# Kernel tuning notes

Hardware: AMD Instinct MI355X
Metric: run time of the kernel (lower is better)

The kernel has to match this reference:

```python
import jax, jax.numpy as jnp
import numpy as np
import math

B, T, C, NH, LEVEL = 2, 2048, 1024, 16, 3


def _build_sets(T, level):
    # hierarchical dyadic sets: levels `level`..floor(log2(T)), step 2^l
    sets = []
    levelmax = int(math.floor(math.log2(T)))
    for l in range(level, levelmax + 1):
        step = 2 ** l
        for i in range(T // step):
            sets.append((i * step, (i + 1) * step - 1))
    b = np.asarray(sets, dtype=np.int32)
    return b[:, 0], b[:, 1]


def setup_inputs() -> dict:
    key = jax.random.key(0)
    kx, kw1, kw2 = jax.random.split(key, 3)
    x = jax.random.normal(kx, (B, T, C), dtype=jnp.float32)
    # torch nn.Linear stores weight as (out_features, in_features); y = x @ W.T
    W_attn = jax.random.normal(kw1, (3 * C, C), dtype=jnp.float32) * (C ** -0.5)
    W_proj = jax.random.normal(kw2, (C, C), dtype=jnp.float32) * (C ** -0.5)
    return {"x": x, "W_attn": W_attn, "W_proj": W_proj}


def _get_slice(xc, l_idx, r_idx):
    # xc: (B,NH,T,hs) cumulative sums; returns sum over [l_idx, r_idx]
    r = xc[:, :, r_idx, :]
    l = xc[:, :, l_idx - 1, :] * (l_idx >= 1)[None, None, :, None].astype(xc.dtype)
    return r - l


def _forward(x, W_attn, W_proj):
    hs = C // NH
    scale = hs ** -0.5
    qkv = x @ W_attn.T                      # (B,T,3C)
    q, k, v = jnp.split(qkv, 3, axis=2)
    heads = lambda t: t.reshape(B, T, NH, hs).transpose(0, 2, 1, 3)  # (B,NH,T,hs)
    q, k, v = heads(q), heads(k), heads(v)
    phi = lambda t: jax.nn.elu(t) + 1.0     # feature_map = 'elu_plus'
    q_phi, k_phi = phi(q), phi(k)
    k_cum = jnp.cumsum(k_phi, axis=2)
    v_cum = jnp.cumsum(v, axis=2)

    l_np, r_np = _build_sets(T, LEVEL)
    l_idx, r_idx = jnp.asarray(l_np), jnp.asarray(r_np)
    K = _get_slice(k_cum, l_idx, r_idx)     # (B,NH,S,hs)
    V = _get_slice(v_cum, l_idx, r_idx)

    t_idx = jnp.arange(T)
    mask = t_idx[:, None] >= r_idx[None, :]                 # (T,S)
    logits = jnp.einsum('bhtd,bhsd->bhts', q, K) * scale    # raw q here (as in source)
    logits = jnp.where(mask[None, None], logits, -jnp.inf)

    # tail term over last (t mod 2^level)+1 tokens, uses q_phi
    Lmin = 2 ** LEVEL
    tail_len = t_idx % Lmin + 1
    l_tail = t_idx - tail_len + 1
    K_tail = _get_slice(k_cum, l_tail, t_idx)               # (B,NH,T,hs)
    V_tail = _get_slice(v_cum, l_tail, t_idx)
    tail_logit = jnp.sum(q_phi * K_tail, axis=-1) * scale   # (B,NH,T)

    full = jnp.concatenate([logits, tail_logit[..., None]], axis=-1)
    att = jax.nn.softmax(full, axis=-1)
    out = jnp.einsum('bhts,bhsd->bhtd', att[..., :-1], V) + att[..., -1:] * V_tail
    out = out.transpose(0, 2, 1, 3).reshape(B, T, C)
    return out @ W_proj.T


def reference(x, W_attn, W_proj):
    return _forward(x, W_attn, W_proj)
```

## Files before the change

### kernel.cpp

```cpp
#include <hip/hip_runtime.h>
#include <hip/hip_bf16.h>
#include <stdint.h>

#define B_    2
#define T_    2048
#define CD    1024
#define NH_   16
#define HS_   64
#define NSETS 511
#define NSP   512
#define QKV_LD 3072
#define NEGBIG (-3.4e38f)
#define QSC   (0.125f * 1.44269504088896f)

typedef __attribute__((ext_vector_type(8))) short  short8;
typedef __attribute__((ext_vector_type(4))) float  f32x4;
typedef _Float16 half8v __attribute__((ext_vector_type(8)));

__device__ __forceinline__ unsigned short f2bf(float f) {
  unsigned u = __float_as_uint(f);
  unsigned r = 0x7FFFu + ((u >> 16) & 1u);
  return (unsigned short)((u + r) >> 16);
}
__device__ __forceinline__ float bf2f(unsigned short h) {
  return __uint_as_float(((unsigned)h) << 16);
}
__device__ __forceinline__ unsigned short f2h(float v) {
  _Float16 h = (_Float16)v;
  return __builtin_bit_cast(unsigned short, h);
}
__device__ __forceinline__ float elu1(float x) {
  return x > 0.f ? x + 1.f : __expf(x);
}
__device__ __forceinline__ void gload16(const unsigned short* g, short* l) {
  __builtin_amdgcn_global_load_lds(
      (const __attribute__((address_space(1))) unsigned int*)g,
      (__attribute__((address_space(3))) unsigned int*)l, 16, 0, 0);
}

__global__ __launch_bounds__(256) void split3_kernel(
    const float* __restrict__ x, const float* __restrict__ Wa,
    const float* __restrict__ Wp,
    unsigned short* __restrict__ xh, unsigned short* __restrict__ xl,
    unsigned short* __restrict__ xf,
    unsigned short* __restrict__ waqh, unsigned short* __restrict__ waql,
    unsigned short* __restrict__ wakvf, unsigned short* __restrict__ wph) {
  int bid = blockIdx.x;
  int t = threadIdx.x;
  if (bid < 16384) {
    int i = bid * 256 + t;
    float v = x[i];
    unsigned short h = f2bf(v);
    xh[i] = h;
    xl[i] = f2bf(v - bf2f(h));
    xf[i] = f2h(v);
  } else if (bid < 20480) {
    int i = (bid - 16384) * 256 + t;
    float v = Wa[i];
    unsigned short h = f2bf(v);
    waqh[i] = h;
    waql[i] = f2bf(v - bf2f(h));
  } else if (bid < 28672) {
    int i = (bid - 20480) * 256 + t;
    wakvf[i] = f2h(Wa[1048576 + i]);
  } else {
    int i = (bid - 28672) * 256 + t;
    wph[i] = f2bf(Wp[i]);
  }
}

template<int SPLIT, int BN, int F16>
__device__ __forceinline__ void gemm_body(
    short* lds,
    const unsigned short* __restrict__ Ah, const unsigned short* __restrict__ Al,
    const unsigned short* __restrict__ Bh, const unsigned short* __restrict__ Bl,
    float* __restrict__ Cmat, int K, int ldc, int row0, int col0)
{
  constexpr int NB   = BN / 16;
  constexpr int ALD  = 8 * (1 + SPLIT);
  constexpr int TL   = ALD + NB * (1 + SPLIT);
  constexpr int PW   = TL / 4;
  constexpr int ASH  = (1 + SPLIT) * 4096;
  constexpr int ABYT = ASH * 2;
  constexpr int NC   = BN / 32;

  const int tid  = threadIdx.x;
  const int lane = tid & 63;
  const int w    = tid >> 6;
  const int wr   = w >> 1, wc = w & 1;

  f32x4 acc[4][NC];
  #pragma unroll
  for (int a = 0; a < 4; ++a)
    #pragma unroll
    for (int b = 0; b < NC; ++b)
      acc[a][b] = (f32x4){0.f, 0.f, 0.f, 0.f};

  const int rlane = lane & 15;
  const int kgrp  = lane >> 4;
  const int rsw   = (kgrp ^ (rlane & 3) ^ ((rlane >> 2) & 3)) << 4;

  const int slr = lane >> 2;
  const int sch = (lane & 3) ^ (slr & 3) ^ ((slr >> 2) & 3);

  for (int kt = 0; kt < K; kt += 32) {
    __syncthreads();
    #pragma unroll
    for (int li = 0; li < PW; ++li) {
      int L = w * PW + li;
      const unsigned short* src; int dsts; size_t rowb;
      if (L < 8)                { src = Ah; rowb = (size_t)row0 + L * 16;       dsts = L * 512; }
      else if (SPLIT && L < 16) { src = Al; rowb = (size_t)row0 + (L - 8) * 16; dsts = 4096 + (L - 8) * 512; }
      else {
        int Lb = L - ALD;
        if (!SPLIT || Lb < NB) { src = Bh; rowb = (size_t)col0 + Lb * 16;        dsts = ASH + Lb * 512; }
        else                   { src = Bl; rowb = (size_t)col0 + (Lb - NB) * 16; dsts = ASH + BN * 32 + (Lb - NB) * 512; }
      }
      gload16(src + (rowb + slr) * K + kt + (sch << 3), lds + dsts + lane * 8);
    }
    __syncthreads();

    short8 aH[4], bH[NC], aL[4], bL[NC];
    #pragma unroll
    for (int m = 0; m < 4; ++m) {
      int r = wr * 64 + m * 16 + rlane;
      aH[m] = *(const short8*)((const char*)lds + r * 64 + rsw);
      if (SPLIT) aL[m] = *(const short8*)((const char*)lds + 8192 + r * 64 + rsw);
    }
    #pragma unroll
    for (int n = 0; n < NC; ++n) {
      int c = wc * (BN / 2) + n * 16 + rlane;
      bH[n] = *(const short8*)((const char*)lds + ABYT + c * 64 + rsw);
      if (SPLIT) bL[n] = *(const short8*)((const char*)lds + ABYT + BN * 64 + c * 64 + rsw);
    }
    #pragma unroll
    for (int mm = 0; mm < 4; ++mm)
      #pragma unroll
      for (int nn = 0; nn < NC; ++nn) {
        if (F16) {
          acc[mm][nn] = __builtin_amdgcn_mfma_f32_16x16x32_f16(
              __builtin_bit_cast(half8v, aH[mm]), __builtin_bit_cast(half8v, bH[nn]),
              acc[mm][nn], 0, 0, 0);
        } else {
          acc[mm][nn] = __builtin_amdgcn_mfma_f32_16x16x32_bf16(aH[mm], bH[nn], acc[mm][nn], 0, 0, 0);
          if (SPLIT) {
            acc[mm][nn] = __builtin_amdgcn_mfma_f32_16x16x32_bf16(aH[mm], bL[nn], acc[mm][nn], 0, 0, 0);
            acc[mm][nn] = __builtin_amdgcn_mfma_f32_16x16x32_bf16(aL[mm], bH[nn], acc[mm][nn], 0, 0, 0);
          }
        }
      }
  }

  const int rl = (lane >> 4) * 4;
  const int cl = lane & 15;
  #pragma unroll
  for (int mm = 0; mm < 4; ++mm)
    #pragma unroll
    for (int nn = 0; nn < NC; ++nn)
      #pragma unroll
      for (int r = 0; r < 4; ++r) {
        int row = row0 + wr * 64 + mm * 16 + rl + r;
        int col = col0 + wc * (BN / 2) + nn * 16 + cl;
        Cmat[(size_t)row * ldc + col] = acc[mm][nn][r];
      }
}

template<int SPLIT, int BN, int F16>
__global__ __launch_bounds__(256) void gemm_bt(
    const unsigned short* __restrict__ Ah, const unsigned short* __restrict__ Al,
    const unsigned short* __restrict__ Bh, const unsigned short* __restrict__ Bl,
    float* __restrict__ Cmat, int M, int N, int K, int ldc)
{
  __shared__ short lds[(1 + SPLIT) * 4096 + (1 + SPLIT) * BN * 32];
  const int nwg = gridDim.x;
  const int cpx = nwg >> 3;
  const int bid = blockIdx.x;
  const int swb = (bid & 7) * cpx + (bid >> 3);
  const int nbx = N / BN;
  const int bx = swb % nbx;
  const int by = swb / nbx;
  gemm_body<SPLIT, BN, F16>(lds, Ah, Al, Bh, Bl, Cmat, K, ldc, by * 128, bx * BN);
}

__global__ __launch_bounds__(256) void cs_part(const float* __restrict__ qkv,
                                               float* __restrict__ part) {
  int blk = blockIdx.x;
  int q   = blk & 1;
  int seg = (blk >> 1) & 127;
  int b   = blk >> 8;
  int c   = threadIdx.x * 4;
  const float* src = qkv + (size_t)(b * T_ + seg * 16) * QKV_LD + CD + q * CD + c;
  float4 s = {0.f, 0.f, 0.f, 0.f};
  #pragma unroll 4
  for (int j = 0; j < 16; ++j) {
    float4 v = *(const float4*)(src + (size_t)j * QKV_LD);
    if (q == 0) {
      s.x += elu1(v.x); s.y += elu1(v.y); s.z += elu1(v.z); s.w += elu1(v.w);
    } else {
      s.x += v.x; s.y += v.y; s.z += v.z; s.w += v.w;
    }
  }
  *(float4*)(part + ((size_t)(b * 128 + seg) * 2048) + q * 1024 + c) = s;
}

__global__ __launch_bounds__(256) void cs_final(const float* __restrict__ qkv,
                                                const float* __restrict__ part,
                                                float* __restrict__ kcum,
                                                float* __restrict__ vcum) {
  int blk = blockIdx.x;
  int q   = blk & 1;
  int seg = (blk >> 1) & 127;
  int b   = blk >> 8;
  int c   = threadIdx.x * 4;
  int h   = c >> 6, d = c & 63;
  float4 s = {0.f, 0.f, 0.f, 0.f};
  const float* pb = part + (size_t)(b * 128) * 2048 + q * 1024 + c;
  #pragma unroll 8
  for (int ss = 0; ss < seg; ++ss) {
    float4 p = *(const float4*)(pb + (size_t)ss * 2048);
    s.x += p.x; s.y += p.y; s.z += p.z; s.w += p.w;
  }
  const float* src = qkv + (size_t)(b * T_ + seg * 16) * QKV_LD + CD + q * CD + c;
  float* dst = (q == 0 ? kcum : vcum) + ((size_t)(b * NH_ + h) * T_ + seg * 16) * HS_ + d;
  #pragma unroll 4
  for (int j = 0; j < 16; ++j) {
    float4 v = *(const float4*)(src + (size_t)j * QKV_LD);
    if (q == 0) {
      s.x += elu1(v.x); s.y += elu1(v.y); s.z += elu1(v.z); s.w += elu1(v.w);
    } else {
      s.x += v.x; s.y += v.y; s.z += v.z; s.w += v.w;
    }
    *(float4*)(dst + (size_t)j * HS_) = s;
  }
}

__global__ __launch_bounds__(256) void build_sets2(
    const float* __restrict__ kcum, const float* __restrict__ vcum,
    unsigned short* __restrict__ Ksh, unsigned short* __restrict__ Ksl,
    unsigned short* __restrict__ Vst, int* __restrict__ r_srt)
{
  __shared__ int   lr[64], lli[64];
  __shared__ float vt[64][65];
  const int bh = blockIdx.x >> 3;
  const int s0 = (blockIdx.x & 7) * 64;
  const int tid = threadIdx.x;

  for (int s = tid; s < NSP; s += 256) {
    int r, li, rank;
    if (s == NSETS) { r = 0x7fffffff; li = 0; rank = NSETS; }
    else {
      int lvl = 3, base = 0;
      while (s >= base + (T_ >> lvl)) { base += T_ >> lvl; ++lvl; }
      int i = s - base;
      int m = (i + 1) << lvl;
      r = m - 1; li = i << lvl;
      rank = lvl - 3;
      #pragma unroll
      for (int j = 3; j <= 11; ++j) rank += (m - 8) >> j;
    }
    if (rank >= s0 && rank < s0 + 64) {
      lr[rank - s0]  = r;
      lli[rank - s0] = li;
      if (bh == 0) r_srt[rank] = r;
    }
  }
  __syncthreads();

  const int sl = tid >> 2;
  const int dq = (tid & 3) * 16;
  const int r  = lr[sl], li = lli[sl];
  const size_t orow = ((size_t)(bh << 9) + s0 + sl) * HS_ + dq;
  short8 kh0, kh1, kl0, kl1;
  if (r == 0x7fffffff) {
    #pragma unroll
    for (int j = 0; j < 8; ++j) { kh0[j]=0; kh1[j]=0; kl0[j]=0; kl1[j]=0; }
    #pragma unroll
    for (int j = 0; j < 16; ++j) vt[sl][dq + j] = 0.f;
  } else {
    const float* kr0 = kcum + ((size_t)bh * T_ + r) * HS_ + dq;
    const float* vr0 = vcum + ((size_t)bh * T_ + r) * HS_ + dq;
    const float* kr1 = kcum + ((size_t)bh * T_ + (li - 1)) * HS_ + dq;
    const float* vr1 = vcum + ((size_t)bh * T_ + (li - 1)) * HS_ + dq;
    #pragma unroll
    for (int g = 0; g < 4; ++g) {
      float4 kv = *(const float4*)(kr0 + g * 4);
      float4 vv = *(const float4*)(vr0 + g * 4);
      if (li > 0) {
        float4 k1 = *(const float4*)(kr1 + g * 4);
        float4 v1 = *(const float4*)(vr1 + g * 4);
        kv.x -= k1.x; kv.y -= k1.y; kv.z -= k1.z; kv.w -= k1.w;
        vv.x -= v1.x; vv.y -= v1.y; vv.z -= v1.z; vv.w -= v1.w;
      }
      float ka[4] = {kv.x, kv.y, kv.z, kv.w};
      float va[4] = {vv.x, vv.y, vv.z, vv.w};
      #pragma unroll
      for (int j = 0; j < 4; ++j) {
        int e = g * 4 + j;
        unsigned short h = f2bf(ka[j]);
        unsigned short l = f2bf(ka[j] - bf2f(h));
        if (e < 8) { kh0[e] = (short)h; kl0[e] = (short)l; }
        else       { kh1[e - 8] = (short)h; kl1[e - 8] = (short)l; }
        vt[sl][dq + e] = va[j];
      }
    }
  }
  *(short8*)(Ksh + orow)     = kh0;
  *(short8*)(Ksh + orow + 8) = kh1;
  *(short8*)(Ksl + orow)     = kl0;
  *(short8*)(Ksl + orow + 8) = kl1;
  __syncthreads();

  const int d  = tid >> 2;
  const int sq = (tid & 3) * 16;
  short8 a, b2;
  #pragma unroll
  for (int j = 0; j < 8; ++j) {
    a[j]  = (short)f2bf(vt[sq + j][d]);
    b2[j] = (short)f2bf(vt[sq + 8 + j][d]);
  }
  unsigned short* dst = Vst + ((size_t)(bh << 6) + d) * NSP + s0 + sq;
  *(short8*)dst = a;
  *(short8*)(dst + 8) = b2;
}

__global__ __launch_bounds__(256) void attn_mfma(
    const float* __restrict__ qkv, const float* __restrict__ kcum,
    const float* __restrict__ vcum,
    const unsigned short* __restrict__ Ksh, const unsigned short* __restrict__ Ksl,
    const unsigned short* __restrict__ Vst, const int* __restrict__ r_srt,
    unsigned short* __restrict__ attnb)
{
  __shared__ short Pl[4 * 1024];
  __shared__ short KV[3 * 4096];
  __shared__ int   rs_lds[NSP];

  const int blk = blockIdx.x;
  const int xcd = blk & 7;
  const int j   = blk >> 3;
  const int bh  = xcd * 4 + (j >> 5);
  const int tch = (j + ((j >> 5) << 3)) & 31;
  const int b = bh >> 4, h = bh & 15;
  const int t0 = tch * 64;
  const int tid = threadIdx.x;
  const int lane = tid & 63;
  const int w = tid >> 6;
  const int col = lane & 15;
  const int kgrp = (lane >> 4) * 8;

  const int srow = lane >> 3;
  const int scsw = ((lane & 7) ^ srow) * 8;

  auto stage_tile = [&](int s0) {
    #pragma unroll
    for (int L = w * 6; L < w * 6 + 6; ++L) {
      int a = L >> 3, i = L & 7;
      const unsigned short* src;
      if (a == 0)      src = Ksh + ((size_t)(bh << 9) + s0 + i * 8 + srow) * 64 + scsw;
      else if (a == 1) src = Ksl + ((size_t)(bh << 9) + s0 + i * 8 + srow) * 64 + scsw;
      else             src = Vst + ((size_t)(bh << 6) + i * 8 + srow) * NSP + s0 + scsw;
      gload16(src, KV + a * 4096 + i * 512 + lane * 8);
    }
  };

  short8 qh[2], ql[2];
  {
    int qrow = t0 + w * 16 + col;
    const float* qr = qkv + (size_t)(b * T_ + qrow) * QKV_LD + h * HS_;
    #pragma unroll
    for (int ks = 0; ks < 2; ++ks) {
      float4 v0 = *(const float4*)(qr + kgrp + ks * 32);
      float4 v1 = *(const float4*)(qr + kgrp + ks * 32 + 4);
      float vv[8] = {v0.x, v0.y, v0.z, v0.w, v1.x, v1.y, v1.z, v1.w};
      #pragma unroll
      for (int jj = 0; jj < 8; ++jj) {
        float sv = vv[jj] * QSC;
        unsigned short hi = f2bf(sv);
        qh[ks][jj] = (short)hi;
        ql[ks][jj] = (short)f2bf(sv - bf2f(hi));
      }
    }
  }
  for (int s = tid; s < NSP; s += 256) rs_lds[s] = r_srt[s];

  int rows[4];
  #pragma unroll
  for (int r = 0; r < 4; ++r) rows[r] = t0 + w * 16 + (lane >> 4) * 4 + r;

  f32x4 O[4];
  float mrun[4], lsum[4];
  #pragma unroll
  for (int f = 0; f < 4; ++f) {
    O[f] = (f32x4){0.f, 0.f, 0.f, 0.f};
    mrun[f] = NEGBIG; lsum[f] = 0.f;
  }

  int nmax = 0;
  #pragma unroll
  for (int jj = 3; jj <= 11; ++jj) nmax += (t0 + 64) >> jj;
  const int ntiles = (nmax + 63) >> 6;

  for (int tile = 0; tile < ntiles; ++tile) {
    const int s0 = tile * 64;
    stage_tile(s0);
    __syncthreads();

    const char* kc = (const char*)KV;
    f32x4 S[4];
    #pragma unroll
    for (int f = 0; f < 4; ++f) S[f] = (f32x4){0.f, 0.f, 0.f, 0.f};

    #pragma unroll
    for (int ks = 0; ks < 2; ++ks) {
      int chnk = (lane >> 4) + ks * 4;
      #pragma unroll
      for (int f = 0; f < 4; ++f) {
        int so = f * 16 + col;
        int kb = so * 128 + ((chnk ^ (so & 7)) << 4);
        short8 bHv = *(const short8*)(kc + kb);
        short8 bLv = *(const short8*)(kc + 8192 + kb);
        S[f] = __builtin_amdgcn_mfma_f32_16x16x32_bf16(qh[ks], bHv, S[f], 0, 0, 0);
        S[f] = __builtin_amdgcn_mfma_f32_16x16x32_bf16(qh[ks], bLv, S[f], 0, 0, 0);
        S[f] = __builtin_amdgcn_mfma_f32_16x16x32_bf16(ql[ks], bHv, S[f], 0, 0, 0);
      }
    }

    int rsv[4];
    #pragma unroll
    for (int f = 0; f < 4; ++f) rsv[f] = rs_lds[s0 + f * 16 + col];

    float zv[4][4];
    #pragma unroll
    for (int f = 0; f < 4; ++f)
      #pragma unroll
      for (int r = 0; r < 4; ++r)
        zv[f][r] = (rsv[f] > rows[r]) ? NEGBIG : S[f][r];

    float mx[4];
    #pragma unroll
    for (int r = 0; r < 4; ++r)
      mx[r] = fmaxf(fmaxf(zv[0][r], zv[1][r]), fmaxf(zv[2][r], zv[3][r]));
    int pred = (mx[0] <= mrun[0] + 11.5f) & (mx[1] <= mrun[1] + 11.5f) &
               (mx[2] <= mrun[2] + 11.5f) & (mx[3] <= mrun[3] + 11.5f);
    if (!__all(pred)) {
      #pragma unroll
      for (int r = 0; r < 4; ++r) {
        float mt = mx[r];
        mt = fmaxf(mt, __shfl_xor(mt, 1));
        mt = fmaxf(mt, __shfl_xor(mt, 2));
        mt = fmaxf(mt, __shfl_xor(mt, 4));
        mt = fmaxf(mt, __shfl_xor(mt, 8));
        float mv = fmaxf(mrun[r], mt);
        float fs = exp2f(mrun[r] - mv);
        lsum[r] *= fs;
        #pragma unroll
        for (int f = 0; f < 4; ++f) O[f][r] *= fs;
        mrun[r] = mv;
      }
    }

    char* pw = (char*)Pl + w * 2048;
    #pragma unroll
    for (int r = 0; r < 4; ++r) {
      int rowr = (lane >> 4) * 4 + r;
      int rswz = (rowr & 7) << 4;
      #pragma unroll
      for (int f = 0; f < 4; ++f) {
        float p = exp2f(zv[f][r] - mrun[r]);
        p = (rsv[f] > rows[r]) ? 0.f : p;
        lsum[r] += p;
        int addr = (rowr * 128 + (f * 16 + col) * 2) ^ rswz;
        *(unsigned short*)(pw + addr) = f2bf(p);
      }
    }

    #pragma unroll
    for (int ks = 0; ks < 2; ++ks) {
      int chnk = (lane >> 4) + ks * 4;
      int pbyte = (col * 128 + (kgrp + ks * 32) * 2) ^ ((col & 7) << 4);
      short8 pa = *(const short8*)(pw + pbyte);
      #pragma unroll
      for (int f = 0; f < 4; ++f) {
        int dr = f * 16 + col;
        short8 bv = *(const short8*)(kc + 16384 + dr * 128 + ((chnk ^ (dr & 7)) << 4));
        O[f] = __builtin_amdgcn_mfma_f32_16x16x32_bf16(pa, bv, O[f], 0, 0, 0);
      }
    }

    __syncthreads();
  }

  float lrun[4];
  #pragma unroll
  for (int r = 0; r < 4; ++r) {
    float l = lsum[r];
    l += __shfl_xor(l, 1);
    l += __shfl_xor(l, 2);
    l += __shfl_xor(l, 4);
    l += __shfl_xor(l, 8);
    lrun[r] = l;
  }

  float ztail;
  {
    int trow = lane >> 2;
    int t = t0 + w * 16 + trow;
    int d0 = (lane & 3) * 16;
    const float* qr = qkv + (size_t)(b * T_ + t) * QKV_LD + h * HS_ + d0;
    float qv[16];
    #pragma unroll
    for (int jj = 0; jj < 4; ++jj) {
      float4 v = *(const float4*)(qr + jj * 4);
      qv[jj*4+0] = v.x; qv[jj*4+1] = v.y; qv[jj*4+2] = v.z; qv[jj*4+3] = v.w;
    }
    int lt = t & ~7;
    const float* kc1 = kcum + ((size_t)bh * T_ + t) * HS_ + d0;
    float kt[16];
    if (lt > 0) {
      const float* kc0 = kcum + ((size_t)bh * T_ + (lt - 1)) * HS_ + d0;
      #pragma unroll
      for (int jj = 0; jj < 16; ++jj) kt[jj] = kc1[jj] - kc0[jj];
    } else {
      #pragma unroll
      for (int jj = 0; jj < 16; ++jj) kt[jj] = kc1[jj];
    }
    float z = 0.f;
    #pragma unroll
    for (int jj = 0; jj < 16; ++jj) {
      float qp = qv[jj] > 0.f ? qv[jj] + 1.f : __expf(qv[jj]);
      z += qp * kt[jj];
    }
    z += __shfl_xor(z, 1);
    z += __shfl_xor(z, 2);
    ztail = z * QSC;
  }

  #pragma unroll
  for (int r = 0; r < 4; ++r) {
    float zt = __shfl(ztail, ((lane >> 4) * 4 + r) * 4);
    float mv = fmaxf(mrun[r], zt);
    float fs = exp2f(mrun[r] - mv);
    float pwgt = exp2f(zt - mv);
    lrun[r] = lrun[r] * fs + pwgt;
    int tr = rows[r];
    int ltr = tr & ~7;
    #pragma unroll
    for (int f = 0; f < 4; ++f) {
      int d = f * 16 + col;
      float v1 = vcum[((size_t)bh * T_ + tr) * HS_ + d];
      float vt = (ltr > 0) ? v1 - vcum[((size_t)bh * T_ + (ltr - 1)) * HS_ + d] : v1;
      O[f][r] = O[f][r] * fs + pwgt * vt;
    }
  }

  #pragma unroll
  for (int r = 0; r < 4; ++r) {
    float inv = 1.f / lrun[r];
    unsigned short* orow = attnb + (size_t)(b * T_ + rows[r]) * CD + h * HS_;
    #pragma unroll
    for (int f = 0; f < 4; ++f)
      orow[f * 16 + col] = f2bf(O[f][r] * inv);
  }
}

extern "C" void kernel_launch(void* const* d_in, const int* in_sizes, int n_in,
                              void* d_out, int out_size, void* d_ws, size_t ws_size,
                              hipStream_t stream) {
  const float* x  = (const float*)d_in[0];
  const float* Wa = (const float*)d_in[1];
  const float* Wp = (const float*)d_in[2];
  float* out = (float*)d_out;

  char* ws = (char*)d_ws;
  size_t off = 0;
  auto alloc = [&](size_t bytes) -> char* {
    char* p = ws + off;
    off += (bytes + 255) & ~(size_t)255;
    return p;
  };

  const int M = B_ * T_;
  float* qkv  = (float*)alloc((size_t)M * QKV_LD * 4);
  float* kcum = (float*)alloc((size_t)B_ * NH_ * T_ * HS_ * 4);
  float* vcum = (float*)alloc((size_t)B_ * NH_ * T_ * HS_ * 4);
  float* part = (float*)alloc((size_t)B_ * 128 * 2048 * 4);
  unsigned short* wph = (unsigned short*)alloc((size_t)CD * CD * 2);

  unsigned short* xf    = (unsigned short*)kcum;
  unsigned short* wakvf = (unsigned short*)vcum;

  char* regionA = alloc((size_t)16777216);
  unsigned short* xh = (unsigned short*)regionA;
  unsigned short* xl = (unsigned short*)(regionA + (size_t)M * CD * 2);
  const size_t SETS_ELEMS = (size_t)B_ * NH_ * NSP * HS_;
  unsigned short* Ksh = (unsigned short*)regionA;
  unsigned short* Ksl = Ksh + SETS_ELEMS;
  unsigned short* Vst = (unsigned short*)(regionA + 2 * SETS_ELEMS * 2);
  int*            r_srt = (int*)(regionA + 3 * SETS_ELEMS * 2);

  char* regionB = alloc((size_t)12582912);
  unsigned short* waqh = (unsigned short*)regionB;
  unsigned short* waql = (unsigned short*)(regionB + (size_t)CD * CD * 2);
  unsigned short* attnb = (unsigned short*)regionB;

  split3_kernel<<<dim3(32768), dim3(256), 0, stream>>>(
      x, Wa, Wp, xh, xl, xf, waqh, waql, wakvf, wph);

  gemm_bt<1, 64, 0><<<dim3(512), dim3(256), 0, stream>>>(
      xh, xl, waqh, waql, qkv, M, 1024, CD, QKV_LD);

  gemm_bt<0, 128, 1><<<dim3(512), dim3(256), 0, stream>>>(
      xf, (const unsigned short*)nullptr, wakvf, (const unsigned short*)nullptr,
      qkv + 1024, M, 2048, CD, QKV_LD);

  cs_part<<<dim3(B_ * 128 * 2), dim3(256), 0, stream>>>(qkv, part);
  cs_final<<<dim3(B_ * 128 * 2), dim3(256), 0, stream>>>(qkv, part, kcum, vcum);

  build_sets2<<<dim3(B_ * NH_ * 8), dim3(256), 0, stream>>>(
      kcum, vcum, Ksh, Ksl, Vst, r_srt);

  attn_mfma<<<dim3(1024), dim3(256), 0, stream>>>(
      qkv, kcum, vcum, Ksh, Ksl, Vst, r_srt, attnb);

  gemm_bt<0, 64, 0><<<dim3(512), dim3(256), 0, stream>>>(
      attnb, (const unsigned short*)nullptr, wph, (const unsigned short*)nullptr,
      out, M, 1024, CD, CD);
}
```

Measured before the change: 185.9 us.

## Split long attention row chunks across two blocks with a combine pass

For the later half of time chunks, which scan more set tiles, the set-tile loop is split between two blocks. Each block writes partial bf16 outputs plus running max and sum, and a new combine kernel merges them with softmax rescaling. The aim is to balance load across the grid and shorten the critical path of the attention kernel. The cost is an extra kernel launch, partial-buffer traffic, and bf16 rounding of the unnormalized partial outputs.

```diff
diff --git a/kernel.cpp b/kernel.cpp
--- a/kernel.cpp
+++ b/kernel.cpp
@@ -328,7 +328,8 @@
     const float* __restrict__ vcum,
     const unsigned short* __restrict__ Ksh, const unsigned short* __restrict__ Ksl,
     const unsigned short* __restrict__ Vst, const int* __restrict__ r_srt,
-    unsigned short* __restrict__ attnb)
+    unsigned short* __restrict__ attnb,
+    unsigned short* __restrict__ pO, float* __restrict__ pm, float* __restrict__ pl)
 {
   __shared__ short Pl[4 * 1024];
   __shared__ short KV[3 * 4096];
@@ -337,8 +338,12 @@
   const int blk = blockIdx.x;
   const int xcd = blk & 7;
   const int j   = blk >> 3;
-  const int bh  = xcd * 4 + (j >> 5);
-  const int tch = (j + ((j >> 5) << 3)) & 31;
+  const int bh  = xcd * 4 + j / 48;
+  const int idx = j % 48;
+  int tch, grp, ngrp;
+  if (idx < 16) { tch = idx; grp = 0; ngrp = 1; }
+  else { int e = idx - 16; tch = 16 + (e >> 1); grp = e & 1; ngrp = 2; }
+
   const int b = bh >> 4, h = bh & 15;
   const int t0 = tch * 64;
   const int tid = threadIdx.x;
@@ -398,8 +403,11 @@
   #pragma unroll
   for (int jj = 3; jj <= 11; ++jj) nmax += (t0 + 64) >> jj;
   const int ntiles = (nmax + 63) >> 6;
-
-  for (int tile = 0; tile < ntiles; ++tile) {
+  const int half   = (ntiles + 1) >> 1;
+  const int tstart = (grp == 0) ? 0 : half;
+  const int tend   = (ngrp == 2 && grp == 0) ? half : ntiles;
+
+  for (int tile = tstart; tile < tend; ++tile) {
     const int s0 = tile * 64;
     stage_tile(s0);
     __syncthreads();
@@ -500,65 +508,120 @@
     lrun[r] = l;
   }
 
-  float ztail;
-  {
-    int trow = lane >> 2;
-    int t = t0 + w * 16 + trow;
-    int d0 = (lane & 3) * 16;
-    const float* qr = qkv + (size_t)(b * T_ + t) * QKV_LD + h * HS_ + d0;
-    float qv[16];
-    #pragma unroll
-    for (int jj = 0; jj < 4; ++jj) {
-      float4 v = *(const float4*)(qr + jj * 4);
-      qv[jj*4+0] = v.x; qv[jj*4+1] = v.y; qv[jj*4+2] = v.z; qv[jj*4+3] = v.w;
-    }
-    int lt = t & ~7;
-    const float* kc1 = kcum + ((size_t)bh * T_ + t) * HS_ + d0;
-    float kt[16];
-    if (lt > 0) {
-      const float* kc0 = kcum + ((size_t)bh * T_ + (lt - 1)) * HS_ + d0;
-      #pragma unroll
-      for (int jj = 0; jj < 16; ++jj) kt[jj] = kc1[jj] - kc0[jj];
-    } else {
-      #pragma unroll
-      for (int jj = 0; jj < 16; ++jj) kt[jj] = kc1[jj];
-    }
-    float z = 0.f;
-    #pragma unroll
-    for (int jj = 0; jj < 16; ++jj) {
-      float qp = qv[jj] > 0.f ? qv[jj] + 1.f : __expf(qv[jj]);
-      z += qp * kt[jj];
-    }
-    z += __shfl_xor(z, 1);
-    z += __shfl_xor(z, 2);
-    ztail = z * QSC;
-  }
-
-  #pragma unroll
-  for (int r = 0; r < 4; ++r) {
-    float zt = __shfl(ztail, ((lane >> 4) * 4 + r) * 4);
-    float mv = fmaxf(mrun[r], zt);
-    float fs = exp2f(mrun[r] - mv);
-    float pwgt = exp2f(zt - mv);
-    lrun[r] = lrun[r] * fs + pwgt;
-    int tr = rows[r];
-    int ltr = tr & ~7;
-    #pragma unroll
-    for (int f = 0; f < 4; ++f) {
-      int d = f * 16 + col;
-      float v1 = vcum[((size_t)bh * T_ + tr) * HS_ + d];
-      float vt = (ltr > 0) ? v1 - vcum[((size_t)bh * T_ + (ltr - 1)) * HS_ + d] : v1;
-      O[f][r] = O[f][r] * fs + pwgt * vt;
-    }
-  }
-
-  #pragma unroll
-  for (int r = 0; r < 4; ++r) {
-    float inv = 1.f / lrun[r];
-    unsigned short* orow = attnb + (size_t)(b * T_ + rows[r]) * CD + h * HS_;
-    #pragma unroll
-    for (int f = 0; f < 4; ++f)
-      orow[f * 16 + col] = f2bf(O[f][r] * inv);
+  if (grp == ngrp - 1) {
+    float ztail;
+    {
+      int trow = lane >> 2;
+      int t = t0 + w * 16 + trow;
+      int d0 = (lane & 3) * 16;
+      const float* qr = qkv + (size_t)(b * T_ + t) * QKV_LD + h * HS_ + d0;
+      float qv[16];
+      #pragma unroll
+      for (int jj = 0; jj < 4; ++jj) {
+        float4 v = *(const float4*)(qr + jj * 4);
+        qv[jj*4+0] = v.x; qv[jj*4+1] = v.y; qv[jj*4+2] = v.z; qv[jj*4+3] = v.w;
+      }
+      int lt = t & ~7;
+      const float* kc1 = kcum + ((size_t)bh * T_ + t) * HS_ + d0;
+      float kt[16];
+      if (lt > 0) {
+        const float* kc0 = kcum + ((size_t)bh * T_ + (lt - 1)) * HS_ + d0;
+        #pragma unroll
+        for (int jj = 0; jj < 16; ++jj) kt[jj] = kc1[jj] - kc0[jj];
+      } else {
+        #pragma unroll
+        for (int jj = 0; jj < 16; ++jj) kt[jj] = kc1[jj];
+      }
+      float z = 0.f;
+      #pragma unroll
+      for (int jj = 0; jj < 16; ++jj) {
+        float qp = qv[jj] > 0.f ? qv[jj] + 1.f : __expf(qv[jj]);
+        z += qp * kt[jj];
+      }
+      z += __shfl_xor(z, 1);
+      z += __shfl_xor(z, 2);
+      ztail = z * QSC;
+    }
+
+    #pragma unroll
+    for (int r = 0; r < 4; ++r) {
+      float zt = __shfl(ztail, ((lane >> 4) * 4 + r) * 4);
+      float mv = fmaxf(mrun[r], zt);
+      float fs = exp2f(mrun[r] - mv);
+      float pwgt = exp2f(zt - mv);
+      lrun[r] = lrun[r] * fs + pwgt;
+      int tr = rows[r];
+      int ltr = tr & ~7;
+      #pragma unroll
+      for (int f = 0; f < 4; ++f) {
+        int d = f * 16 + col;
+        float v1 = vcum[((size_t)bh * T_ + tr) * HS_ + d];
+        float vt = (ltr > 0) ? v1 - vcum[((size_t)bh * T_ + (ltr - 1)) * HS_ + d] : v1;
+        O[f][r] = O[f][r] * fs + pwgt * vt;
+      }
+      mrun[r] = mv;
+    }
+  }
+
+  if (ngrp == 1) {
+    #pragma unroll
+    for (int r = 0; r < 4; ++r) {
+      float inv = 1.f / lrun[r];
+      unsigned short* orow = attnb + (size_t)(b * T_ + rows[r]) * CD + h * HS_;
+      #pragma unroll
+      for (int f = 0; f < 4; ++f)
+        orow[f * 16 + col] = f2bf(O[f][r] * inv);
+    }
+  } else {
+    const int pidx = (((bh << 4) + (tch - 16)) << 1) + grp;
+    #pragma unroll
+    for (int r = 0; r < 4; ++r) {
+      int lrow = w * 16 + (lane >> 4) * 4 + r;
+      unsigned short* prow = pO + (size_t)pidx * 4096 + lrow * 64;
+      #pragma unroll
+      for (int f = 0; f < 4; ++f)
+        prow[f * 16 + col] = f2bf(O[f][r]);
+      if (col == 0) {
+        pm[pidx * 64 + lrow] = mrun[r];
+        pl[pidx * 64 + lrow] = lrun[r];
+      }
+    }
+  }
+}
+
+__global__ __launch_bounds__(256) void combine(
+    const unsigned short* __restrict__ pO, const float* __restrict__ pm,
+    const float* __restrict__ pl, unsigned short* __restrict__ attnb)
+{
+  int blk = blockIdx.x;
+  int bh = blk >> 4, tc = blk & 15;
+  int b = bh >> 4, h = bh & 15;
+  int tch = 16 + tc;
+  int tid = threadIdx.x;
+  int row = tid >> 2;
+  int d0  = (tid & 3) * 16;
+  int p0 = (((bh << 4) + tc) << 1), p1 = p0 + 1;
+
+  float m0 = pm[p0 * 64 + row], l0 = pl[p0 * 64 + row];
+  float m1 = pm[p1 * 64 + row], l1 = pl[p1 * 64 + row];
+  float m  = fmaxf(m0, m1);
+  float w0 = exp2f(m0 - m), w1 = exp2f(m1 - m);
+  float linv = 1.f / (l0 * w0 + l1 * w1);
+
+  const unsigned short* o0 = pO + (size_t)p0 * 4096 + row * 64 + d0;
+  const unsigned short* o1 = pO + (size_t)p1 * 4096 + row * 64 + d0;
+  unsigned short* orow = attnb + (size_t)(b * T_ + tch * 64 + row) * CD + h * HS_ + d0;
+  short8 a0 = *(const short8*)o0, a1 = *(const short8*)o1;
+  short8 b0 = *(const short8*)(o0 + 8), b1 = *(const short8*)(o1 + 8);
+  #pragma unroll
+  for (int jj = 0; jj < 8; ++jj) {
+    float v = bf2f((unsigned short)a0[jj]) * w0 + bf2f((unsigned short)a1[jj]) * w1;
+    orow[jj] = f2bf(v * linv);
+  }
+  #pragma unroll
+  for (int jj = 0; jj < 8; ++jj) {
+    float v = bf2f((unsigned short)b0[jj]) * w0 + bf2f((unsigned short)b1[jj]) * w1;
+    orow[8 + jj] = f2bf(v * linv);
   }
 }
 
@@ -596,6 +659,9 @@
   unsigned short* Ksl = Ksh + SETS_ELEMS;
   unsigned short* Vst = (unsigned short*)(regionA + 2 * SETS_ELEMS * 2);
   int*            r_srt = (int*)(regionA + 3 * SETS_ELEMS * 2);
+  float*          pm  = (float*)(regionA + 3 * SETS_ELEMS * 2 + 4096);
+  float*          pl  = (float*)(regionA + 3 * SETS_ELEMS * 2 + 4096 + 262144);
+  unsigned short* pO  = (unsigned short*)(regionA + (size_t)8 * 1048576);
 
   char* regionB = alloc((size_t)12582912);
   unsigned short* waqh = (unsigned short*)regionB;
@@ -618,8 +684,10 @@
   build_sets2<<<dim3(B_ * NH_ * 8), dim3(256), 0, stream>>>(
       kcum, vcum, Ksh, Ksl, Vst, r_srt);
 
-  attn_mfma<<<dim3(1024), dim3(256), 0, stream>>>(
-      qkv, kcum, vcum, Ksh, Ksl, Vst, r_srt, attnb);
+  attn_mfma<<<dim3(1536), dim3(256), 0, stream>>>(
+      qkv, kcum, vcum, Ksh, Ksl, Vst, r_srt, attnb, pO, pm, pl);
+
+  combine<<<dim3(512), dim3(256), 0, stream>>>(pO, pm, pl, attnb);
 
   gemm_bt<0, 64, 0><<<dim3(512), dim3(256), 0, stream>>>(
       attnb, (const unsigned short*)nullptr, wph, (const unsigned short*)nullptr,
```

Measured after the change: 189.7 us. +2.1%, slower.

## Process two 16-row query groups per wave in attention kernel with 128 threads

Applied to the files above, without the earlier changes.

The attention kernel now runs 2 waves per block instead of 4, and each wave handles 32 query rows as two 16-row sub-tiles. Each K/V fragment read from LDS then feeds twice as many MFMAs, which cuts LDS read traffic per FLOP. Each wave also stages twice as many tile loads. The cost is roughly double the accumulator and softmax registers per thread, which can lower occupancy. Fewer waves per block also leaves less latency hiding around the per-tile barriers. The redundant masking select on p was dropped because masked logits already underflow to zero.

```diff
diff --git a/kernel.cpp b/kernel.cpp
--- a/kernel.cpp
+++ b/kernel.cpp
@@ -323,14 +323,14 @@
   *(short8*)(dst + 8) = b2;
 }
 
-__global__ __launch_bounds__(256) void attn_mfma(
+__global__ __launch_bounds__(128) void attn_mfma(
     const float* __restrict__ qkv, const float* __restrict__ kcum,
     const float* __restrict__ vcum,
     const unsigned short* __restrict__ Ksh, const unsigned short* __restrict__ Ksl,
     const unsigned short* __restrict__ Vst, const int* __restrict__ r_srt,
     unsigned short* __restrict__ attnb)
 {
-  __shared__ short Pl[4 * 1024];
+  __shared__ short Pl[2 * 2048];
   __shared__ short KV[3 * 4096];
   __shared__ int   rs_lds[NSP];
 
@@ -352,7 +352,7 @@
 
   auto stage_tile = [&](int s0) {
     #pragma unroll
-    for (int L = w * 6; L < w * 6 + 6; ++L) {
+    for (int L = w * 12; L < w * 12 + 12; ++L) {
       int a = L >> 3, i = L & 7;
       const unsigned short* src;
       if (a == 0)      src = Ksh + ((size_t)(bh << 9) + s0 + i * 8 + srow) * 64 + scsw;
@@ -362,9 +362,10 @@
     }
   };
 
-  short8 qh[2], ql[2];
-  {
-    int qrow = t0 + w * 16 + col;
+  short8 qh[2][2], ql[2][2];
+  #pragma unroll
+  for (int rr = 0; rr < 2; ++rr) {
+    int qrow = t0 + w * 32 + rr * 16 + col;
     const float* qr = qkv + (size_t)(b * T_ + qrow) * QKV_LD + h * HS_;
     #pragma unroll
     for (int ks = 0; ks < 2; ++ks) {
@@ -375,24 +376,29 @@
       for (int jj = 0; jj < 8; ++jj) {
         float sv = vv[jj] * QSC;
         unsigned short hi = f2bf(sv);
-        qh[ks][jj] = (short)hi;
-        ql[ks][jj] = (short)f2bf(sv - bf2f(hi));
-      }
-    }
-  }
-  for (int s = tid; s < NSP; s += 256) rs_lds[s] = r_srt[s];
-
-  int rows[4];
-  #pragma unroll
-  for (int r = 0; r < 4; ++r) rows[r] = t0 + w * 16 + (lane >> 4) * 4 + r;
-
-  f32x4 O[4];
-  float mrun[4], lsum[4];
-  #pragma unroll
-  for (int f = 0; f < 4; ++f) {
-    O[f] = (f32x4){0.f, 0.f, 0.f, 0.f};
-    mrun[f] = NEGBIG; lsum[f] = 0.f;
-  }
+        qh[rr][ks][jj] = (short)hi;
+        ql[rr][ks][jj] = (short)f2bf(sv - bf2f(hi));
+      }
+    }
+  }
+  for (int s = tid; s < NSP; s += 128) rs_lds[s] = r_srt[s];
+
+  int rows[2][4];
+  #pragma unroll
+  for (int rr = 0; rr < 2; ++rr)
+    #pragma unroll
+    for (int r = 0; r < 4; ++r)
+      rows[rr][r] = t0 + w * 32 + rr * 16 + (lane >> 4) * 4 + r;
+
+  f32x4 O[2][4];
+  float mrun[2][4], lsum[2][4];
+  #pragma unroll
+  for (int rr = 0; rr < 2; ++rr)
+    #pragma unroll
+    for (int f = 0; f < 4; ++f) {
+      O[rr][f] = (f32x4){0.f, 0.f, 0.f, 0.f};
+      mrun[rr][f] = NEGBIG; lsum[rr][f] = 0.f;
+    }
 
   int nmax = 0;
   #pragma unroll
@@ -405,9 +411,11 @@
     __syncthreads();
 
     const char* kc = (const char*)KV;
-    f32x4 S[4];
-    #pragma unroll
-    for (int f = 0; f < 4; ++f) S[f] = (f32x4){0.f, 0.f, 0.f, 0.f};
+    f32x4 S[2][4];
+    #pragma unroll
+    for (int rr = 0; rr < 2; ++rr)
+      #pragma unroll
+      for (int f = 0; f < 4; ++f) S[rr][f] = (f32x4){0.f, 0.f, 0.f, 0.f};
 
     #pragma unroll
     for (int ks = 0; ks < 2; ++ks) {
@@ -418,9 +426,12 @@
         int kb = so * 128 + ((chnk ^ (so & 7)) << 4);
         short8 bHv = *(const short8*)(kc + kb);
         short8 bLv = *(const short8*)(kc + 8192 + kb);
-        S[f] = __builtin_amdgcn_mfma_f32_16x16x32_bf16(qh[ks], bHv, S[f], 0, 0, 0);
-        S[f] = __builtin_amdgcn_mfma_f32_16x16x32_bf16(qh[ks], bLv, S[f], 0, 0, 0);
-        S[f] = __builtin_amdgcn_mfma_f32_16x16x32_bf16(ql[ks], bHv, S[f], 0, 0, 0);
+        #pragma unroll
+        for (int rr = 0; rr < 2; ++rr) {
+          S[rr][f] = __builtin_amdgcn_mfma_f32_16x16x32_bf16(qh[rr][ks], bHv, S[rr][f], 0, 0, 0);
+          S[rr][f] = __builtin_amdgcn_mfma_f32_16x16x32_bf16(qh[rr][ks], bLv, S[rr][f], 0, 0, 0);
+          S[rr][f] = __builtin_amdgcn_mfma_f32_16x16x32_bf16(ql[rr][ks], bHv, S[rr][f], 0, 0, 0);
+        }
       }
     }
 
@@ -428,82 +439,96 @@
     #pragma unroll
     for (int f = 0; f < 4; ++f) rsv[f] = rs_lds[s0 + f * 16 + col];
 
-    float zv[4][4];
-    #pragma unroll
-    for (int f = 0; f < 4; ++f)
-      #pragma unroll
-      for (int r = 0; r < 4; ++r)
-        zv[f][r] = (rsv[f] > rows[r]) ? NEGBIG : S[f][r];
-
-    float mx[4];
-    #pragma unroll
-    for (int r = 0; r < 4; ++r)
-      mx[r] = fmaxf(fmaxf(zv[0][r], zv[1][r]), fmaxf(zv[2][r], zv[3][r]));
-    int pred = (mx[0] <= mrun[0] + 11.5f) & (mx[1] <= mrun[1] + 11.5f) &
-               (mx[2] <= mrun[2] + 11.5f) & (mx[3] <= mrun[3] + 11.5f);
+    float zv[2][4][4];
+    #pragma unroll
+    for (int rr = 0; rr < 2; ++rr)
+      #pragma unroll
+      for (int f = 0; f < 4; ++f)
+        #pragma unroll
+        for (int r = 0; r < 4; ++r)
+          zv[rr][f][r] = (rsv[f] > rows[rr][r]) ? NEGBIG : S[rr][f][r];
+
+    float mx[2][4];
+    int pred = 1;
+    #pragma unroll
+    for (int rr = 0; rr < 2; ++rr)
+      #pragma unroll
+      for (int r = 0; r < 4; ++r) {
+        mx[rr][r] = fmaxf(fmaxf(zv[rr][0][r], zv[rr][1][r]),
+                          fmaxf(zv[rr][2][r], zv[rr][3][r]));
+        pred &= (mx[rr][r] <= mrun[rr][r] + 11.5f);
+      }
     if (!__all(pred)) {
       #pragma unroll
+      for (int rr = 0; rr < 2; ++rr)
+        #pragma unroll
+        for (int r = 0; r < 4; ++r) {
+          float mt = mx[rr][r];
+          mt = fmaxf(mt, __shfl_xor(mt, 1));
+          mt = fmaxf(mt, __shfl_xor(mt, 2));
+          mt = fmaxf(mt, __shfl_xor(mt, 4));
+          mt = fmaxf(mt, __shfl_xor(mt, 8));
+          float mv = fmaxf(mrun[rr][r], mt);
+          float fs = exp2f(mrun[rr][r] - mv);
+          lsum[rr][r] *= fs;
+          #pragma unroll
+          for (int f = 0; f < 4; ++f) O[rr][f][r] *= fs;
+          mrun[rr][r] = mv;
+        }
+    }
+
+    char* pw = (char*)Pl + w * 4096;
+    #pragma unroll
+    for (int rr = 0; rr < 2; ++rr)
+      #pragma unroll
       for (int r = 0; r < 4; ++r) {
-        float mt = mx[r];
-        mt = fmaxf(mt, __shfl_xor(mt, 1));
-        mt = fmaxf(mt, __shfl_xor(mt, 2));
-        mt = fmaxf(mt, __shfl_xor(mt, 4));
-        mt = fmaxf(mt, __shfl_xor(mt, 8));
-        float mv = fmaxf(mrun[r], mt);
-        float fs = exp2f(mrun[r] - mv);
-        lsum[r] *= fs;
+        int rowr = rr * 16 + (lane >> 4) * 4 + r;
+        int rswz = (rowr & 7) << 4;
         #pragma unroll
-        for (int f = 0; f < 4; ++f) O[f][r] *= fs;
-        mrun[r] = mv;
-      }
-    }
-
-    char* pw = (char*)Pl + w * 2048;
-    #pragma unroll
-    for (int r = 0; r < 4; ++r) {
-      int rowr = (lane >> 4) * 4 + r;
-      int rswz = (rowr & 7) << 4;
-      #pragma unroll
-      for (int f = 0; f < 4; ++f) {
-        float p = exp2f(zv[f][r] - mrun[r]);
-        p = (rsv[f] > rows[r]) ? 0.f : p;
-        lsum[r] += p;
-        int addr = (rowr * 128 + (f * 16 + col) * 2) ^ rswz;
-        *(unsigned short*)(pw + addr) = f2bf(p);
-      }
-    }
+        for (int f = 0; f < 4; ++f) {
+          float p = exp2f(zv[rr][f][r] - mrun[rr][r]);
+          lsum[rr][r] += p;
+          int addr = (rowr * 128 + (f * 16 + col) * 2) ^ rswz;
+          *(unsigned short*)(pw + addr) = f2bf(p);
+        }
+      }
 
     #pragma unroll
     for (int ks = 0; ks < 2; ++ks) {
       int chnk = (lane >> 4) + ks * 4;
-      int pbyte = (col * 128 + (kgrp + ks * 32) * 2) ^ ((col & 7) << 4);
-      short8 pa = *(const short8*)(pw + pbyte);
+      int pb0 = (col * 128 + (kgrp + ks * 32) * 2) ^ ((col & 7) << 4);
+      short8 pa0 = *(const short8*)(pw + pb0);
+      short8 pa1 = *(const short8*)(pw + 2048 + pb0);
       #pragma unroll
       for (int f = 0; f < 4; ++f) {
         int dr = f * 16 + col;
         short8 bv = *(const short8*)(kc + 16384 + dr * 128 + ((chnk ^ (dr & 7)) << 4));
-        O[f] = __builtin_amdgcn_mfma_f32_16x16x32_bf16(pa, bv, O[f], 0, 0, 0);
+        O[0][f] = __builtin_amdgcn_mfma_f32_16x16x32_bf16(pa0, bv, O[0][f], 0, 0, 0);
+        O[1][f] = __builtin_amdgcn_mfma_f32_16x16x32_bf16(pa1, bv, O[1][f], 0, 0, 0);
       }
     }
 
     __syncthreads();
   }
 
-  float lrun[4];
-  #pragma unroll
-  for (int r = 0; r < 4; ++r) {
-    float l = lsum[r];
-    l += __shfl_xor(l, 1);
-    l += __shfl_xor(l, 2);
-    l += __shfl_xor(l, 4);
-    l += __shfl_xor(l, 8);
-    lrun[r] = l;
-  }
-
-  float ztail;
-  {
+  float lrun[2][4];
+  #pragma unroll
+  for (int rr = 0; rr < 2; ++rr)
+    #pragma unroll
+    for (int r = 0; r < 4; ++r) {
+      float l = lsum[rr][r];
+      l += __shfl_xor(l, 1);
+      l += __shfl_xor(l, 2);
+      l += __shfl_xor(l, 4);
+      l += __shfl_xor(l, 8);
+      lrun[rr][r] = l;
+    }
+
+  float ztail[2];
+  #pragma unroll
+  for (int rr = 0; rr < 2; ++rr) {
     int trow = lane >> 2;
-    int t = t0 + w * 16 + trow;
+    int t = t0 + w * 32 + rr * 16 + trow;
     int d0 = (lane & 3) * 16;
     const float* qr = qkv + (size_t)(b * T_ + t) * QKV_LD + h * HS_ + d0;
     float qv[16];
@@ -531,35 +556,39 @@
     }
     z += __shfl_xor(z, 1);
     z += __shfl_xor(z, 2);
-    ztail = z * QSC;
-  }
-
-  #pragma unroll
-  for (int r = 0; r < 4; ++r) {
-    float zt = __shfl(ztail, ((lane >> 4) * 4 + r) * 4);
-    float mv = fmaxf(mrun[r], zt);
-    float fs = exp2f(mrun[r] - mv);
-    float pwgt = exp2f(zt - mv);
-    lrun[r] = lrun[r] * fs + pwgt;
-    int tr = rows[r];
-    int ltr = tr & ~7;
-    #pragma unroll
-    for (int f = 0; f < 4; ++f) {
-      int d = f * 16 + col;
-      float v1 = vcum[((size_t)bh * T_ + tr) * HS_ + d];
-      float vt = (ltr > 0) ? v1 - vcum[((size_t)bh * T_ + (ltr - 1)) * HS_ + d] : v1;
-      O[f][r] = O[f][r] * fs + pwgt * vt;
-    }
-  }
-
-  #pragma unroll
-  for (int r = 0; r < 4; ++r) {
-    float inv = 1.f / lrun[r];
-    unsigned short* orow = attnb + (size_t)(b * T_ + rows[r]) * CD + h * HS_;
-    #pragma unroll
-    for (int f = 0; f < 4; ++f)
-      orow[f * 16 + col] = f2bf(O[f][r] * inv);
-  }
+    ztail[rr] = z * QSC;
+  }
+
+  #pragma unroll
+  for (int rr = 0; rr < 2; ++rr)
+    #pragma unroll
+    for (int r = 0; r < 4; ++r) {
+      float zt = __shfl(ztail[rr], ((lane >> 4) * 4 + r) * 4);
+      float mv = fmaxf(mrun[rr][r], zt);
+      float fs = exp2f(mrun[rr][r] - mv);
+      float pwgt = exp2f(zt - mv);
+      lrun[rr][r] = lrun[rr][r] * fs + pwgt;
+      int tr = rows[rr][r];
+      int ltr = tr & ~7;
+      #pragma unroll
+      for (int f = 0; f < 4; ++f) {
+        int d = f * 16 + col;
+        float v1 = vcum[((size_t)bh * T_ + tr) * HS_ + d];
+        float vt = (ltr > 0) ? v1 - vcum[((size_t)bh * T_ + (ltr - 1)) * HS_ + d] : v1;
+        O[rr][f][r] = O[rr][f][r] * fs + pwgt * vt;
+      }
+    }
+
+  #pragma unroll
+  for (int rr = 0; rr < 2; ++rr)
+    #pragma unroll
+    for (int r = 0; r < 4; ++r) {
+      float inv = 1.f / lrun[rr][r];
+      unsigned short* orow = attnb + (size_t)(b * T_ + rows[rr][r]) * CD + h * HS_;
+      #pragma unroll
+      for (int f = 0; f < 4; ++f)
+        orow[f * 16 + col] = f2bf(O[rr][f][r] * inv);
+    }
 }
 
 extern "C" void kernel_launch(void* const* d_in, const int* in_sizes, int n_in,
@@ -618,7 +647,7 @@
   build_sets2<<<dim3(B_ * NH_ * 8), dim3(256), 0, stream>>>(
       kcum, vcum, Ksh, Ksl, Vst, r_srt);
 
-  attn_mfma<<<dim3(1024), dim3(256), 0, stream>>>(
+  attn_mfma<<<dim3(1024), dim3(128), 0, stream>>>(
       qkv, kcum, vcum, Ksh, Ksl, Vst, r_srt, attnb);
 
   gemm_bt<0, 64, 0><<<dim3(512), dim3(256), 0, stream>>>(
```

Result: slower. 205.7 us (+10.7%).
